# Kernel optimization log

Hardware: AMD Instinct MI355X
Metric: run time of the kernel (lower is better)

Reference implementation:

```python
import jax, jax.numpy as jnp
import numpy as np

N = 50000      # nodes
E = 800000     # edges
F_IN = 10      # node_feat_dim
H = 64         # hidden
ED = 3         # edge_dim
L = 3          # num_layers
EPS_LN = 1e-5


def _layernorm(x, g, b):
    mu = jnp.mean(x, axis=-1, keepdims=True)
    var = jnp.mean((x - mu) ** 2, axis=-1, keepdims=True)
    return (x - mu) * jax.lax.rsqrt(var + EPS_LN) * g + b


def setup_inputs() -> dict:
    key = jax.random.key(0)
    ks = jax.random.split(key, 20)
    x = jax.random.normal(ks[0], (N, F_IN), dtype=jnp.float32)
    edge_index = jax.random.randint(ks[1], (2, E), 0, N, dtype=jnp.int32)
    edge_attr = jax.random.uniform(ks[2], (E, ED), dtype=jnp.float32)

    def lin(k, fan_in, shape):
        return jax.random.normal(k, shape, dtype=jnp.float32) / np.sqrt(fan_in)

    params = {
        "Wp": lin(ks[3], F_IN, (F_IN, H)),
        "bp": jnp.zeros((H,), jnp.float32),
        # per-layer stacked params, leading dim L
        "ew1": lin(ks[4], ED, (L, ED, 16)),
        "eb1": jnp.zeros((L, 16), jnp.float32),
        "ew2": lin(ks[5], 16, (L, 16, 1)),
        "eb2": jnp.zeros((L, 1), jnp.float32),
        "nw": lin(ks[6], 2 * H, (L, 2 * H, H)),
        "nb": jnp.zeros((L, H), jnp.float32),
        "ln_g": jnp.ones((L, H), jnp.float32),
        "ln_b": jnp.zeros((L, H), jnp.float32),
        "hw1": lin(ks[7], H, (H, H // 2)),
        "hb1": jnp.zeros((H // 2,), jnp.float32),
        "hw2": lin(ks[8], H // 2, (H // 2, 1)),
        "hb2": jnp.zeros((1,), jnp.float32),
    }
    return {"x": x, "edge_index": edge_index, "edge_attr": edge_attr, **params}


def reference(x, edge_index, edge_attr, Wp, bp, ew1, eb1, ew2, eb2,
              nw, nb, ln_g, ln_b, hw1, hb1, hw2, hb2):
    src, dst = edge_index[0], edge_index[1]
    h = jax.nn.relu(x @ Wp + bp)                       # (N, H)
    for l in range(L):
        # edge MLP -> sigmoid weight per edge, shape (E, 1)
        ew = jax.nn.sigmoid(jax.nn.relu(edge_attr @ ew1[l] + eb1[l]) @ ew2[l] + eb2[l])
        msg = h[src] * ew                              # (E, H) gather + scale
        agg = jax.ops.segment_sum(msg, dst, num_segments=N)   # (N, H)
        cnt = jax.ops.segment_sum(ew, dst, num_segments=N)    # (N, 1)
        agg = agg / jnp.maximum(cnt, 1e-12)
        upd = jax.nn.relu(jnp.concatenate([h, agg], axis=1) @ nw[l] + nb[l])
        h = _layernorm(h + upd, ln_g[l], ln_b[l])
    return jax.nn.relu(h @ hw1 + hb1) @ hw2 + hb2      # (N, 1) logits
```

## Files before the change

kernel.cpp:

```cpp
#include <hip/hip_runtime.h>
#include <math.h>

#define N_NODES 50000
#define N_EDGES 800000
#define N_STRIPS 3125
#define N_BUCKETS 196
#define CAP_B 6144
#define CHUNK_A 2048
#define FILLA_BLOCKS 391
#define PROJ_BLOCKS 12500

typedef __attribute__((ext_vector_type(8))) short bf16x8;
typedef __attribute__((ext_vector_type(4))) float f32x4;
typedef __attribute__((ext_vector_type(2))) float f32x2;

__device__ __forceinline__ unsigned short f2bf(float f) {
  unsigned int u = __float_as_uint(f);
  u += 0x7FFFu + ((u >> 16) & 1u);
  return (unsigned short)(u >> 16);
}
__device__ __forceinline__ float bf2f(unsigned short s) {
  return __uint_as_float(((unsigned int)s) << 16);
}
__device__ __forceinline__ unsigned char f2fp8(float f) {
  return (unsigned char)(__builtin_amdgcn_cvt_pk_fp8_f32(f, f, 0, false) & 0xFF);
}

__global__ __launch_bounds__(256) void k_pre(const int* __restrict__ ei,
                                             const float* __restrict__ ea,
                                             const float* __restrict__ ew1,
                                             const float* __restrict__ eb1,
                                             const float* __restrict__ ew2,
                                             const float* __restrict__ eb2,
                                             int* __restrict__ bcur,
                                             uint2* __restrict__ buf1,
                                             const float* __restrict__ x,
                                             const float* __restrict__ Wp,
                                             const float* __restrict__ bp,
                                             unsigned short* __restrict__ hb,
                                             unsigned char* __restrict__ h8) {
  __shared__ int lcnt[N_BUCKETS];
  __shared__ int gb[N_BUCKETS];
  if (blockIdx.x >= FILLA_BLOCKS) {
    int idx = (blockIdx.x - FILLA_BLOCKS) * 256 + threadIdx.x;
    int n = idx >> 6, j = idx & 63;
    float acc = bp[j];
#pragma unroll
    for (int k = 0; k < 10; k++) acc += __builtin_nontemporal_load(&x[n * 10 + k]) * Wp[k * 64 + j];
    float r = fmaxf(acc, 0.f);
    hb[n * 64 + j] = f2bf(r);
    h8[n * 64 + j] = f2fp8(r);
    return;
  }
  for (int i = threadIdx.x; i < N_BUCKETS; i += 256) lcnt[i] = 0;
  __syncthreads();
  int base = blockIdx.x * CHUNK_A;
  uint2 rec[CHUNK_A / 256];
  int bk[CHUNK_A / 256], rk[CHUNK_A / 256];
#pragma unroll
  for (int k = 0; k < CHUNK_A / 256; k++) {
    int e = base + k * 256 + threadIdx.x;
    bk[k] = -1;
    if (e < N_EDGES) {
      int s = __builtin_nontemporal_load(&ei[e]);
      int d = __builtin_nontemporal_load(&ei[N_EDGES + e]);
      float a0 = __builtin_nontemporal_load(&ea[e * 3 + 0]);
      float a1 = __builtin_nontemporal_load(&ea[e * 3 + 1]);
      float a2 = __builtin_nontemporal_load(&ea[e * 3 + 2]);
      int q[3];
#pragma unroll
      for (int l = 0; l < 3; l++) {
        float z = eb2[l];
#pragma unroll
        for (int t = 0; t < 16; t++) {
          float hd = a0 * ew1[l * 48 + t] + a1 * ew1[l * 48 + 16 + t] +
                     a2 * ew1[l * 48 + 32 + t] + eb1[l * 16 + t];
          z += fmaxf(hd, 0.f) * ew2[l * 16 + t];
        }
        float w = 1.f / (1.f + __expf(-z));
        q[l] = __float2int_rn(w * 8191.f);
      }
      unsigned int dl = (unsigned int)(d & 255);
      rec[k].x = (unsigned int)s | ((unsigned int)q[0] << 17) | ((dl & 3u) << 30);
      rec[k].y = (unsigned int)q[1] | ((unsigned int)q[2] << 13) | ((dl >> 2) << 26);
      int b = d >> 8;
      bk[k] = b;
      rk[k] = atomicAdd(&lcnt[b], 1);
    }
  }
  __syncthreads();
  if (threadIdx.x < N_BUCKETS) {
    int c = lcnt[threadIdx.x];
    gb[threadIdx.x] = threadIdx.x * CAP_B + (c ? atomicAdd(&bcur[threadIdx.x], c) : 0);
  }
  __syncthreads();
#pragma unroll
  for (int k = 0; k < CHUNK_A / 256; k++)
    if (bk[k] >= 0) buf1[gb[bk[k]] + rk[k]] = rec[k];
}

__global__ __launch_bounds__(256) void k_fillB(const uint2* __restrict__ buf1,
                                               const int* __restrict__ bcur,
                                               uint2* __restrict__ csr,
                                               int* __restrict__ aoffs,
                                               int* __restrict__ adeg,
                                               int* __restrict__ order) {
  __shared__ int lhist[256];
  __shared__ int lscan[256];
  __shared__ int lcls[8];
  __shared__ int lbase[8];
  int b = blockIdx.x;
  int t = threadIdx.x;
  int segbase = b * CAP_B;
  int cnt = bcur[b];
  lhist[t] = 0;
  if (t < 8) lcls[t] = 0;
  __syncthreads();
  for (int i = t; i < cnt; i += 256) {
    uint2 rec = buf1[segbase + i];
    int dl = (int)((rec.x >> 30) | (((rec.y >> 26) & 63u) << 2));
    atomicAdd(&lhist[dl], 1);
  }
  __syncthreads();
  int v = lhist[t];
  lscan[t] = v;
  __syncthreads();
#pragma unroll
  for (int off = 1; off < 256; off <<= 1) {
    int u = (t >= off) ? lscan[t - off] : 0;
    __syncthreads();
    lscan[t] += u;
    __syncthreads();
  }
  int excl = lscan[t] - v;
  int nid = b * 256 + t;
  int cls = 0, rank = 0;
  bool valid = nid < N_NODES;
  if (valid) {
    aoffs[nid] = segbase + excl;
    adeg[nid] = v;
    cls = min(v >> 2, 7);
    rank = atomicAdd(&lcls[cls], 1);
  }
  __syncthreads();
  if (t == 0) {
    int acc2 = 0;
#pragma unroll
    for (int c = 0; c < 8; c++) { lbase[c] = acc2; acc2 += lcls[c]; }
  }
  lhist[t] = segbase + excl;
  __syncthreads();
  if (valid) order[b * 256 + lbase[cls] + rank] = nid;
  for (int i = t; i < cnt; i += 256) {
    uint2 rec = buf1[segbase + i];
    int dl = (int)((rec.x >> 30) | (((rec.y >> 26) & 63u) << 2));
    int pos = atomicAdd(&lhist[dl], 1);
    csr[pos] = rec;
  }
}

template <int LI>
__device__ __forceinline__ float decw(uint2 c) {
  unsigned int q = (LI == 0) ? ((c.x >> 17) & 0x1FFFu)
                 : (LI == 1) ? (c.y & 0x1FFFu)
                             : ((c.y >> 13) & 0x1FFFu);
  return (float)q * (1.f / 8191.f);
}

template <int LI>
__global__ __launch_bounds__(256, 8) void k_agg(const uint2* __restrict__ csr,
                                                const int* __restrict__ aoffs,
                                                const int* __restrict__ adeg,
                                                const int* __restrict__ order,
                                                const unsigned char* __restrict__ h8in,
                                                unsigned short* __restrict__ ab) {
  int lane = threadIdx.x & 63;
  int sub = lane >> 3;
  int jj = lane & 7;
  int gw = (blockIdx.x * 256 + threadIdx.x) >> 6;
  int idx = gw * 8 + sub;
  bool active = idx < N_NODES;
  int n = active ? order[idx] : 0;
  int start = active ? aoffs[n] : 0;
  int d = active ? adeg[n] : 0;
  const uint2* hrow = (const uint2*)h8in;
  float a0 = 0.f, a1 = 0.f, a2 = 0.f, a3 = 0.f;
  float a4 = 0.f, a5 = 0.f, a6 = 0.f, a7 = 0.f, ws = 0.f;
  int i = 0;
  if (d >= 4) {
    uint2 c0 = csr[start + 0], c1 = csr[start + 1];
    uint2 c2 = csr[start + 2], c3 = csr[start + 3];
    for (;;) {
      int nxt = i + 4;
      bool more = (nxt + 4 <= d);
      uint2 m0, m1, m2, m3;
      if (more) {
        m0 = csr[start + nxt + 0]; m1 = csr[start + nxt + 1];
        m2 = csr[start + nxt + 2]; m3 = csr[start + nxt + 3];
      }
      uint2 g0 = hrow[(c0.x & 0x1FFFFu) * 8 + jj];
      uint2 g1 = hrow[(c1.x & 0x1FFFFu) * 8 + jj];
      uint2 g2 = hrow[(c2.x & 0x1FFFFu) * 8 + jj];
      uint2 g3 = hrow[(c3.x & 0x1FFFFu) * 8 + jj];
      float w0 = decw<LI>(c0), w1 = decw<LI>(c1), w2 = decw<LI>(c2), w3 = decw<LI>(c3);
#pragma unroll
      for (int k = 0; k < 4; k++) {
        uint2 g = (k == 0) ? g0 : (k == 1) ? g1 : (k == 2) ? g2 : g3;
        float w = (k == 0) ? w0 : (k == 1) ? w1 : (k == 2) ? w2 : w3;
        f32x2 p01 = __builtin_amdgcn_cvt_pk_f32_fp8(g.x, false);
        f32x2 p23 = __builtin_amdgcn_cvt_pk_f32_fp8(g.x, true);
        f32x2 p45 = __builtin_amdgcn_cvt_pk_f32_fp8(g.y, false);
        f32x2 p67 = __builtin_amdgcn_cvt_pk_f32_fp8(g.y, true);
        a0 += p01[0] * w; a1 += p01[1] * w;
        a2 += p23[0] * w; a3 += p23[1] * w;
        a4 += p45[0] * w; a5 += p45[1] * w;
        a6 += p67[0] * w; a7 += p67[1] * w;
      }
      ws += w0 + w1 + w2 + w3;
      i = nxt;
      if (!more) break;
      c0 = m0; c1 = m1; c2 = m2; c3 = m3;
    }
  }
  for (; i < d; ++i) {
    uint2 c = csr[start + i];
    uint2 g = hrow[(c.x & 0x1FFFFu) * 8 + jj];
    float w = decw<LI>(c);
    f32x2 p01 = __builtin_amdgcn_cvt_pk_f32_fp8(g.x, false);
    f32x2 p23 = __builtin_amdgcn_cvt_pk_f32_fp8(g.x, true);
    f32x2 p45 = __builtin_amdgcn_cvt_pk_f32_fp8(g.y, false);
    f32x2 p67 = __builtin_amdgcn_cvt_pk_f32_fp8(g.y, true);
    a0 += p01[0] * w; a1 += p01[1] * w;
    a2 += p23[0] * w; a3 += p23[1] * w;
    a4 += p45[0] * w; a5 += p45[1] * w;
    a6 += p67[0] * w; a7 += p67[1] * w;
    ws += w;
  }
  if (active) {
    float inv = 1.f / fmaxf(ws, 1e-12f);
    uint4 o;
    o.x = (unsigned int)f2bf(a0 * inv) | ((unsigned int)f2bf(a1 * inv) << 16);
    o.y = (unsigned int)f2bf(a2 * inv) | ((unsigned int)f2bf(a3 * inv) << 16);
    o.z = (unsigned int)f2bf(a4 * inv) | ((unsigned int)f2bf(a5 * inv) << 16);
    o.w = (unsigned int)f2bf(a6 * inv) | ((unsigned int)f2bf(a7 * inv) << 16);
    ((uint4*)ab)[n * 8 + jj] = o;
  }
}

template <bool HEAD>
__global__ __launch_bounds__(256) void k_mlp(const float* __restrict__ nw,
                                             const float* __restrict__ nb,
                                             const float* __restrict__ g,
                                             const float* __restrict__ b,
                                             const unsigned short* __restrict__ hb_in,
                                             const unsigned short* __restrict__ ab_in,
                                             unsigned short* __restrict__ hbout,
                                             unsigned char* __restrict__ h8out,
                                             const float* __restrict__ hw1,
                                             const float* __restrict__ hb1,
                                             const float* __restrict__ hw2,
                                             const float* __restrict__ hb2,
                                             float* __restrict__ out) {
  __shared__ unsigned short lh[4][16 * 72];
  int lane = threadIdx.x & 63;
  int n16 = lane & 15;
  int q = lane >> 4;
  int wv = threadIdx.x >> 6;
  int wid = (blockIdx.x * 256 + threadIdx.x) >> 6;
  int nwaves = gridDim.x * 4;

  bf16x8 bfr[4][4];
#pragma unroll
  for (int t = 0; t < 4; t++)
#pragma unroll
    for (int kc = 0; kc < 4; kc++) {
      bf16x8 v;
#pragma unroll
      for (int jj = 0; jj < 8; jj++) {
        int k = kc * 32 + q * 8 + jj;
        v[jj] = (short)f2bf(nw[k * 64 + t * 16 + n16]);
      }
      bfr[t][kc] = v;
    }
  bf16x8 eye[2];
#pragma unroll
  for (int p = 0; p < 2; p++) {
    bf16x8 v;
#pragma unroll
    for (int jj = 0; jj < 8; jj++)
      v[jj] = ((q * 8 + jj) == (n16 + 16 * p)) ? (short)0x3F80 : (short)0;
    eye[p] = v;
  }
  float nbv[4], gv[4], bv[4];
#pragma unroll
  for (int t = 0; t < 4; t++) {
    nbv[t] = nb[t * 16 + n16];
    gv[t] = g[t * 16 + n16];
    bv[t] = b[t * 16 + n16];
  }
  bf16x8 hfr[2][2];
  float hb1v[2], hw2v[2], hb2v = 0.f;
  if (HEAD) {
#pragma unroll
    for (int kc = 0; kc < 2; kc++)
#pragma unroll
      for (int tl = 0; tl < 2; tl++) {
        bf16x8 v;
#pragma unroll
        for (int jj = 0; jj < 8; jj++)
          v[jj] = (short)f2bf(hw1[(kc * 32 + q * 8 + jj) * 32 + tl * 16 + n16]);
        hfr[kc][tl] = v;
      }
#pragma unroll
    for (int tl = 0; tl < 2; tl++) {
      hb1v[tl] = hb1[tl * 16 + n16];
      hw2v[tl] = hw2[tl * 16 + n16];
    }
    hb2v = hb2[0];
  }

  for (int s = wid; s < N_STRIPS; s += nwaves) {
    int n0 = s * 16;
    f32x4 acc[4] = {{0.f, 0.f, 0.f, 0.f}, {0.f, 0.f, 0.f, 0.f},
                    {0.f, 0.f, 0.f, 0.f}, {0.f, 0.f, 0.f, 0.f}};
    bf16x8 afr[4];
#pragma unroll
    for (int kc = 0; kc < 4; kc++) {
      const unsigned short* base = (kc < 2) ? hb_in : ab_in;
      afr[kc] = __builtin_nontemporal_load(
          (const bf16x8*)(base + (size_t)(n0 + n16) * 64 + (kc & 1) * 32 + q * 8));
#pragma unroll
      for (int t = 0; t < 4; t++)
        acc[t] = __builtin_amdgcn_mfma_f32_16x16x32_bf16(afr[kc], bfr[t][kc], acc[t], 0, 0, 0);
    }
    f32x4 rres[4];
#pragma unroll
    for (int t = 0; t < 4; t++) {
      f32x4 z = {0.f, 0.f, 0.f, 0.f};
      rres[t] = __builtin_amdgcn_mfma_f32_16x16x32_bf16(afr[t >> 1], eye[t & 1], z, 0, 0, 0);
    }
    float r[4][4];
    float p[4], p2[4];
#pragma unroll
    for (int rg = 0; rg < 4; rg++) { p[rg] = 0.f; p2[rg] = 0.f; }
#pragma unroll
    for (int t = 0; t < 4; t++)
#pragma unroll
      for (int rg = 0; rg < 4; rg++) {
        float rr = rres[t][rg] + fmaxf(acc[t][rg] + nbv[t], 0.f);
        r[t][rg] = rr;
        p[rg] += rr;
        p2[rg] += rr * rr;
      }
#pragma unroll
    for (int rg = 0; rg < 4; rg++)
#pragma unroll
      for (int off = 1; off < 16; off <<= 1) {
        p[rg] += __shfl_xor(p[rg], off);
        p2[rg] += __shfl_xor(p2[rg], off);
      }
#pragma unroll
    for (int rg = 0; rg < 4; rg++) {
      float mu = p[rg] * (1.f / 64.f);
      float var = p2[rg] * (1.f / 64.f) - mu * mu;
      float rs = rsqrtf(fmaxf(var, 0.f) + 1e-5f);
      int row = n0 + q * 4 + rg;
#pragma unroll
      for (int t = 0; t < 4; t++) {
        float o = (r[t][rg] - mu) * rs * gv[t] + bv[t];
        unsigned short ob = f2bf(o);
        hbout[row * 64 + t * 16 + n16] = ob;
        h8out[row * 64 + t * 16 + n16] = f2fp8(o);
        if (HEAD) lh[wv][(q * 4 + rg) * 72 + t * 16 + n16] = ob;
      }
    }
    if (HEAD) {
      asm volatile("s_waitcnt lgkmcnt(0)" ::: "memory");
      f32x4 hacc[2] = {{0.f, 0.f, 0.f, 0.f}, {0.f, 0.f, 0.f, 0.f}};
#pragma unroll
      for (int kc = 0; kc < 2; kc++) {
        bf16x8 ha = *(const bf16x8*)&lh[wv][n16 * 72 + kc * 32 + q * 8];
#pragma unroll
        for (int tl = 0; tl < 2; tl++)
          hacc[tl] = __builtin_amdgcn_mfma_f32_16x16x32_bf16(ha, hfr[kc][tl], hacc[tl], 0, 0, 0);
      }
#pragma unroll
      for (int rg = 0; rg < 4; rg++) {
        float sres = fmaxf(hacc[0][rg] + hb1v[0], 0.f) * hw2v[0] +
                     fmaxf(hacc[1][rg] + hb1v[1], 0.f) * hw2v[1];
#pragma unroll
        for (int off = 1; off < 16; off <<= 1) sres += __shfl_xor(sres, off);
        if (n16 == 0) out[n0 + q * 4 + rg] = sres + hb2v;
      }
    }
  }
}

static inline size_t align256(size_t x) { return (x + 255) & ~size_t(255); }

extern "C" void kernel_launch(void* const* d_in, const int* in_sizes, int n_in,
                              void* d_out, int out_size, void* d_ws, size_t ws_size,
                              hipStream_t stream) {
  const float* x   = (const float*)d_in[0];
  const int*   ei  = (const int*)d_in[1];
  const float* ea  = (const float*)d_in[2];
  const float* Wp  = (const float*)d_in[3];
  const float* bp  = (const float*)d_in[4];
  const float* ew1 = (const float*)d_in[5];
  const float* eb1 = (const float*)d_in[6];
  const float* ew2 = (const float*)d_in[7];
  const float* eb2 = (const float*)d_in[8];
  const float* nw  = (const float*)d_in[9];
  const float* nb  = (const float*)d_in[10];
  const float* lng = (const float*)d_in[11];
  const float* lnb = (const float*)d_in[12];
  const float* hw1 = (const float*)d_in[13];
  const float* hb1 = (const float*)d_in[14];
  const float* hw2 = (const float*)d_in[15];
  const float* hb2 = (const float*)d_in[16];
  float* out = (float*)d_out;

  char* ws = (char*)d_ws;
  size_t off = 0;
  unsigned short* hb0  = (unsigned short*)(ws + off); off = align256(off + (size_t)N_NODES * 64 * 2);
  unsigned short* hb1b = (unsigned short*)(ws + off); off = align256(off + (size_t)N_NODES * 64 * 2);
  unsigned short* ab   = (unsigned short*)(ws + off); off = align256(off + (size_t)N_NODES * 64 * 2);
  unsigned char* h8_0  = (unsigned char*)(ws + off); off = align256(off + (size_t)N_NODES * 64);
  unsigned char* h8_1  = (unsigned char*)(ws + off); off = align256(off + (size_t)N_NODES * 64);
  uint2* csr  = (uint2*)(ws + off); off = align256(off + (size_t)N_BUCKETS * CAP_B * 8);
  uint2* buf1 = (uint2*)(ws + off); off = align256(off + (size_t)N_BUCKETS * CAP_B * 8);
  int* aoffs  = (int*)(ws + off); off = align256(off + (size_t)N_NODES * 4);
  int* adeg   = (int*)(ws + off); off = align256(off + (size_t)N_NODES * 4);
  int* order  = (int*)(ws + off); off = align256(off + (size_t)N_NODES * 4);
  int* bcur   = (int*)(ws + off); off = align256(off + 1024);

  (void)hipMemsetAsync(bcur, 0, N_BUCKETS * 4, stream);
  k_pre<<<FILLA_BLOCKS + PROJ_BLOCKS, 256, 0, stream>>>(ei, ea, ew1, eb1, ew2, eb2, bcur, buf1,
                                                        x, Wp, bp, hb0, h8_0);
  k_fillB<<<N_BUCKETS, 256, 0, stream>>>(buf1, bcur, csr, aoffs, adeg, order);

  const int aggGrid = (N_NODES + 31) / 32;
  const int mlpGrid = 392;

  k_agg<0><<<aggGrid, 256, 0, stream>>>(csr, aoffs, adeg, order, h8_0, ab);
  k_mlp<false><<<mlpGrid, 256, 0, stream>>>(nw + 0 * 8192, nb + 0 * 64, lng + 0 * 64, lnb + 0 * 64,
                                            hb0, ab, hb1b, h8_1, hw1, hb1, hw2, hb2, out);
  k_agg<1><<<aggGrid, 256, 0, stream>>>(csr, aoffs, adeg, order, h8_1, ab);
  k_mlp<false><<<mlpGrid, 256, 0, stream>>>(nw + 1 * 8192, nb + 1 * 64, lng + 1 * 64, lnb + 1 * 64,
                                            hb1b, ab, hb0, h8_0, hw1, hb1, hw2, hb2, out);
  k_agg<2><<<aggGrid, 256, 0, stream>>>(csr, aoffs, adeg, order, h8_0, ab);
  k_mlp<true><<<mlpGrid, 256, 0, stream>>>(nw + 2 * 8192, nb + 2 * 64, lng + 2 * 64, lnb + 2 * 64,
                                           hb0, ab, hb1b, h8_1, hw1, hb1, hw2, hb2, out);
}
```

Before: 220.6 us.

## Fuse neighbor aggregation into node-update MLP kernel and split CSR per layer

Merges the per-layer aggregation kernel and the MLP/LayerNorm kernel into one persistent kernel. Each wave aggregates 16 degree-sorted nodes into shared memory and feeds them straight into the MFMA update, which removes the bf16 aggregate round trip through global memory and half the launches. The CSR records are also repacked into three 4-byte per-layer arrays (source index plus that layer's quantized weight) instead of one 8-byte record, halving edge-stream bytes per layer. In exchange, node rows are now read and written in degree-sorted scattered order, and occupancy is limited by the launch bound of 3 blocks.

```diff
diff --git a/kernel.cpp b/kernel.cpp
--- a/kernel.cpp
+++ b/kernel.cpp
@@ -18,9 +18,6 @@
   unsigned int u = __float_as_uint(f);
   u += 0x7FFFu + ((u >> 16) & 1u);
   return (unsigned short)(u >> 16);
-}
-__device__ __forceinline__ float bf2f(unsigned short s) {
-  return __uint_as_float(((unsigned int)s) << 16);
 }
 __device__ __forceinline__ unsigned char f2fp8(float f) {
   return (unsigned char)(__builtin_amdgcn_cvt_pk_fp8_f32(f, f, 0, false) & 0xFF);
@@ -101,7 +98,9 @@
 
 __global__ __launch_bounds__(256) void k_fillB(const uint2* __restrict__ buf1,
                                                const int* __restrict__ bcur,
-                                               uint2* __restrict__ csr,
+                                               unsigned int* __restrict__ pl0,
+                                               unsigned int* __restrict__ pl1,
+                                               unsigned int* __restrict__ pl2,
                                                int* __restrict__ aoffs,
                                                int* __restrict__ adeg,
                                                int* __restrict__ order) {
@@ -155,180 +154,170 @@
     uint2 rec = buf1[segbase + i];
     int dl = (int)((rec.x >> 30) | (((rec.y >> 26) & 63u) << 2));
     int pos = atomicAdd(&lhist[dl], 1);
-    csr[pos] = rec;
-  }
-}
-
-template <int LI>
-__device__ __forceinline__ float decw(uint2 c) {
-  unsigned int q = (LI == 0) ? ((c.x >> 17) & 0x1FFFu)
-                 : (LI == 1) ? (c.y & 0x1FFFu)
-                             : ((c.y >> 13) & 0x1FFFu);
-  return (float)q * (1.f / 8191.f);
-}
-
-template <int LI>
-__global__ __launch_bounds__(256, 8) void k_agg(const uint2* __restrict__ csr,
-                                                const int* __restrict__ aoffs,
-                                                const int* __restrict__ adeg,
-                                                const int* __restrict__ order,
-                                                const unsigned char* __restrict__ h8in,
-                                                unsigned short* __restrict__ ab) {
+    unsigned int src = rec.x & 0x1FFFFu;
+    pl0[pos] = src | ((rec.x >> 17) & 0x1FFFu) << 17;
+    pl1[pos] = src | (rec.y & 0x1FFFu) << 17;
+    pl2[pos] = src | ((rec.y >> 13) & 0x1FFFu) << 17;
+  }
+}
+
+template <bool HEAD>
+__global__ __launch_bounds__(256, 3) void k_layer(
+    const unsigned int* __restrict__ pl,
+    const int* __restrict__ aoffs,
+    const int* __restrict__ adeg,
+    const int* __restrict__ order,
+    const unsigned char* __restrict__ h8in,
+    const unsigned short* __restrict__ hb_in,
+    const float* __restrict__ nw, const float* __restrict__ nb,
+    const float* __restrict__ g, const float* __restrict__ b,
+    unsigned short* __restrict__ hbout, unsigned char* __restrict__ h8out,
+    const float* __restrict__ hw1, const float* __restrict__ hb1,
+    const float* __restrict__ hw2, const float* __restrict__ hb2,
+    float* __restrict__ out) {
+  __shared__ unsigned short lt[4][16 * 72];
   int lane = threadIdx.x & 63;
+  int n16 = lane & 15;
+  int q = lane >> 4;
   int sub = lane >> 3;
   int jj = lane & 7;
-  int gw = (blockIdx.x * 256 + threadIdx.x) >> 6;
-  int idx = gw * 8 + sub;
-  bool active = idx < N_NODES;
-  int n = active ? order[idx] : 0;
-  int start = active ? aoffs[n] : 0;
-  int d = active ? adeg[n] : 0;
+  int wv = threadIdx.x >> 6;
+  int wid = (blockIdx.x * 256 + threadIdx.x) >> 6;
+  int nwaves = gridDim.x * 4;
+
+  bf16x8 bfr[4][4];
+#pragma unroll
+  for (int t = 0; t < 4; t++)
+#pragma unroll
+    for (int kc = 0; kc < 4; kc++) {
+      bf16x8 v;
+#pragma unroll
+      for (int j2 = 0; j2 < 8; j2++) {
+        int k = kc * 32 + q * 8 + j2;
+        v[j2] = (short)f2bf(nw[k * 64 + t * 16 + n16]);
+      }
+      bfr[t][kc] = v;
+    }
+  bf16x8 eye[2];
+#pragma unroll
+  for (int p = 0; p < 2; p++) {
+    bf16x8 v;
+#pragma unroll
+    for (int j2 = 0; j2 < 8; j2++)
+      v[j2] = ((q * 8 + j2) == (n16 + 16 * p)) ? (short)0x3F80 : (short)0;
+    eye[p] = v;
+  }
+  float nbv[4], gv[4], bv[4];
+#pragma unroll
+  for (int t = 0; t < 4; t++) {
+    nbv[t] = nb[t * 16 + n16];
+    gv[t] = g[t * 16 + n16];
+    bv[t] = b[t * 16 + n16];
+  }
+  bf16x8 hfr[2][2];
+  float hb1v[2], hw2v[2], hb2v = 0.f;
+  if (HEAD) {
+#pragma unroll
+    for (int kc = 0; kc < 2; kc++)
+#pragma unroll
+      for (int tl = 0; tl < 2; tl++) {
+        bf16x8 v;
+#pragma unroll
+        for (int j2 = 0; j2 < 8; j2++)
+          v[j2] = (short)f2bf(hw1[(kc * 32 + q * 8 + j2) * 32 + tl * 16 + n16]);
+        hfr[kc][tl] = v;
+      }
+#pragma unroll
+    for (int tl = 0; tl < 2; tl++) {
+      hb1v[tl] = hb1[tl * 16 + n16];
+      hw2v[tl] = hw2[tl * 16 + n16];
+    }
+    hb2v = hb2[0];
+  }
+
   const uint2* hrow = (const uint2*)h8in;
-  float a0 = 0.f, a1 = 0.f, a2 = 0.f, a3 = 0.f;
-  float a4 = 0.f, a5 = 0.f, a6 = 0.f, a7 = 0.f, ws = 0.f;
-  int i = 0;
-  if (d >= 4) {
-    uint2 c0 = csr[start + 0], c1 = csr[start + 1];
-    uint2 c2 = csr[start + 2], c3 = csr[start + 3];
-    for (;;) {
-      int nxt = i + 4;
-      bool more = (nxt + 4 <= d);
-      uint2 m0, m1, m2, m3;
-      if (more) {
-        m0 = csr[start + nxt + 0]; m1 = csr[start + nxt + 1];
-        m2 = csr[start + nxt + 2]; m3 = csr[start + nxt + 3];
-      }
-      uint2 g0 = hrow[(c0.x & 0x1FFFFu) * 8 + jj];
-      uint2 g1 = hrow[(c1.x & 0x1FFFFu) * 8 + jj];
-      uint2 g2 = hrow[(c2.x & 0x1FFFFu) * 8 + jj];
-      uint2 g3 = hrow[(c3.x & 0x1FFFFu) * 8 + jj];
-      float w0 = decw<LI>(c0), w1 = decw<LI>(c1), w2 = decw<LI>(c2), w3 = decw<LI>(c3);
-#pragma unroll
-      for (int k = 0; k < 4; k++) {
-        uint2 g = (k == 0) ? g0 : (k == 1) ? g1 : (k == 2) ? g2 : g3;
-        float w = (k == 0) ? w0 : (k == 1) ? w1 : (k == 2) ? w2 : w3;
-        f32x2 p01 = __builtin_amdgcn_cvt_pk_f32_fp8(g.x, false);
-        f32x2 p23 = __builtin_amdgcn_cvt_pk_f32_fp8(g.x, true);
-        f32x2 p45 = __builtin_amdgcn_cvt_pk_f32_fp8(g.y, false);
-        f32x2 p67 = __builtin_amdgcn_cvt_pk_f32_fp8(g.y, true);
+
+  for (int s = wid; s < N_STRIPS; s += nwaves) {
+#pragma unroll
+    for (int half = 0; half < 2; half++) {
+      int n = order[s * 16 + half * 8 + sub];
+      int start = aoffs[n];
+      int d = adeg[n];
+      float a0 = 0.f, a1 = 0.f, a2 = 0.f, a3 = 0.f;
+      float a4 = 0.f, a5 = 0.f, a6 = 0.f, a7 = 0.f, ws = 0.f;
+      int i = 0;
+      if (d >= 4) {
+        unsigned int c0 = pl[start + 0], c1 = pl[start + 1];
+        unsigned int c2 = pl[start + 2], c3 = pl[start + 3];
+        for (;;) {
+          int nxt = i + 4;
+          bool more = (nxt + 4 <= d);
+          unsigned int m0, m1, m2, m3;
+          if (more) {
+            m0 = pl[start + nxt + 0]; m1 = pl[start + nxt + 1];
+            m2 = pl[start + nxt + 2]; m3 = pl[start + nxt + 3];
+          }
+          uint2 g0 = hrow[(c0 & 0x1FFFFu) * 8 + jj];
+          uint2 g1 = hrow[(c1 & 0x1FFFFu) * 8 + jj];
+          uint2 g2 = hrow[(c2 & 0x1FFFFu) * 8 + jj];
+          uint2 g3 = hrow[(c3 & 0x1FFFFu) * 8 + jj];
+          float w0 = (float)(c0 >> 17) * (1.f / 8191.f);
+          float w1 = (float)(c1 >> 17) * (1.f / 8191.f);
+          float w2 = (float)(c2 >> 17) * (1.f / 8191.f);
+          float w3 = (float)(c3 >> 17) * (1.f / 8191.f);
+#pragma unroll
+          for (int k = 0; k < 4; k++) {
+            uint2 gg = (k == 0) ? g0 : (k == 1) ? g1 : (k == 2) ? g2 : g3;
+            float w = (k == 0) ? w0 : (k == 1) ? w1 : (k == 2) ? w2 : w3;
+            f32x2 p01 = __builtin_amdgcn_cvt_pk_f32_fp8(gg.x, false);
+            f32x2 p23 = __builtin_amdgcn_cvt_pk_f32_fp8(gg.x, true);
+            f32x2 p45 = __builtin_amdgcn_cvt_pk_f32_fp8(gg.y, false);
+            f32x2 p67 = __builtin_amdgcn_cvt_pk_f32_fp8(gg.y, true);
+            a0 += p01[0] * w; a1 += p01[1] * w;
+            a2 += p23[0] * w; a3 += p23[1] * w;
+            a4 += p45[0] * w; a5 += p45[1] * w;
+            a6 += p67[0] * w; a7 += p67[1] * w;
+          }
+          ws += w0 + w1 + w2 + w3;
+          i = nxt;
+          if (!more) break;
+          c0 = m0; c1 = m1; c2 = m2; c3 = m3;
+        }
+      }
+      for (; i < d; ++i) {
+        unsigned int c = pl[start + i];
+        uint2 gg = hrow[(c & 0x1FFFFu) * 8 + jj];
+        float w = (float)(c >> 17) * (1.f / 8191.f);
+        f32x2 p01 = __builtin_amdgcn_cvt_pk_f32_fp8(gg.x, false);
+        f32x2 p23 = __builtin_amdgcn_cvt_pk_f32_fp8(gg.x, true);
+        f32x2 p45 = __builtin_amdgcn_cvt_pk_f32_fp8(gg.y, false);
+        f32x2 p67 = __builtin_amdgcn_cvt_pk_f32_fp8(gg.y, true);
         a0 += p01[0] * w; a1 += p01[1] * w;
         a2 += p23[0] * w; a3 += p23[1] * w;
         a4 += p45[0] * w; a5 += p45[1] * w;
         a6 += p67[0] * w; a7 += p67[1] * w;
-      }
-      ws += w0 + w1 + w2 + w3;
-      i = nxt;
-      if (!more) break;
-      c0 = m0; c1 = m1; c2 = m2; c3 = m3;
-    }
-  }
-  for (; i < d; ++i) {
-    uint2 c = csr[start + i];
-    uint2 g = hrow[(c.x & 0x1FFFFu) * 8 + jj];
-    float w = decw<LI>(c);
-    f32x2 p01 = __builtin_amdgcn_cvt_pk_f32_fp8(g.x, false);
-    f32x2 p23 = __builtin_amdgcn_cvt_pk_f32_fp8(g.x, true);
-    f32x2 p45 = __builtin_amdgcn_cvt_pk_f32_fp8(g.y, false);
-    f32x2 p67 = __builtin_amdgcn_cvt_pk_f32_fp8(g.y, true);
-    a0 += p01[0] * w; a1 += p01[1] * w;
-    a2 += p23[0] * w; a3 += p23[1] * w;
-    a4 += p45[0] * w; a5 += p45[1] * w;
-    a6 += p67[0] * w; a7 += p67[1] * w;
-    ws += w;
-  }
-  if (active) {
-    float inv = 1.f / fmaxf(ws, 1e-12f);
-    uint4 o;
-    o.x = (unsigned int)f2bf(a0 * inv) | ((unsigned int)f2bf(a1 * inv) << 16);
-    o.y = (unsigned int)f2bf(a2 * inv) | ((unsigned int)f2bf(a3 * inv) << 16);
-    o.z = (unsigned int)f2bf(a4 * inv) | ((unsigned int)f2bf(a5 * inv) << 16);
-    o.w = (unsigned int)f2bf(a6 * inv) | ((unsigned int)f2bf(a7 * inv) << 16);
-    ((uint4*)ab)[n * 8 + jj] = o;
-  }
-}
-
-template <bool HEAD>
-__global__ __launch_bounds__(256) void k_mlp(const float* __restrict__ nw,
-                                             const float* __restrict__ nb,
-                                             const float* __restrict__ g,
-                                             const float* __restrict__ b,
-                                             const unsigned short* __restrict__ hb_in,
-                                             const unsigned short* __restrict__ ab_in,
-                                             unsigned short* __restrict__ hbout,
-                                             unsigned char* __restrict__ h8out,
-                                             const float* __restrict__ hw1,
-                                             const float* __restrict__ hb1,
-                                             const float* __restrict__ hw2,
-                                             const float* __restrict__ hb2,
-                                             float* __restrict__ out) {
-  __shared__ unsigned short lh[4][16 * 72];
-  int lane = threadIdx.x & 63;
-  int n16 = lane & 15;
-  int q = lane >> 4;
-  int wv = threadIdx.x >> 6;
-  int wid = (blockIdx.x * 256 + threadIdx.x) >> 6;
-  int nwaves = gridDim.x * 4;
-
-  bf16x8 bfr[4][4];
-#pragma unroll
-  for (int t = 0; t < 4; t++)
-#pragma unroll
-    for (int kc = 0; kc < 4; kc++) {
-      bf16x8 v;
-#pragma unroll
-      for (int jj = 0; jj < 8; jj++) {
-        int k = kc * 32 + q * 8 + jj;
-        v[jj] = (short)f2bf(nw[k * 64 + t * 16 + n16]);
-      }
-      bfr[t][kc] = v;
-    }
-  bf16x8 eye[2];
-#pragma unroll
-  for (int p = 0; p < 2; p++) {
-    bf16x8 v;
-#pragma unroll
-    for (int jj = 0; jj < 8; jj++)
-      v[jj] = ((q * 8 + jj) == (n16 + 16 * p)) ? (short)0x3F80 : (short)0;
-    eye[p] = v;
-  }
-  float nbv[4], gv[4], bv[4];
-#pragma unroll
-  for (int t = 0; t < 4; t++) {
-    nbv[t] = nb[t * 16 + n16];
-    gv[t] = g[t * 16 + n16];
-    bv[t] = b[t * 16 + n16];
-  }
-  bf16x8 hfr[2][2];
-  float hb1v[2], hw2v[2], hb2v = 0.f;
-  if (HEAD) {
-#pragma unroll
-    for (int kc = 0; kc < 2; kc++)
-#pragma unroll
-      for (int tl = 0; tl < 2; tl++) {
-        bf16x8 v;
-#pragma unroll
-        for (int jj = 0; jj < 8; jj++)
-          v[jj] = (short)f2bf(hw1[(kc * 32 + q * 8 + jj) * 32 + tl * 16 + n16]);
-        hfr[kc][tl] = v;
-      }
-#pragma unroll
-    for (int tl = 0; tl < 2; tl++) {
-      hb1v[tl] = hb1[tl * 16 + n16];
-      hw2v[tl] = hw2[tl * 16 + n16];
-    }
-    hb2v = hb2[0];
-  }
-
-  for (int s = wid; s < N_STRIPS; s += nwaves) {
-    int n0 = s * 16;
+        ws += w;
+      }
+      float inv = 1.f / fmaxf(ws, 1e-12f);
+      unsigned int u0 = (unsigned int)f2bf(a0 * inv) | ((unsigned int)f2bf(a1 * inv) << 16);
+      unsigned int u1 = (unsigned int)f2bf(a2 * inv) | ((unsigned int)f2bf(a3 * inv) << 16);
+      unsigned int u2 = (unsigned int)f2bf(a4 * inv) | ((unsigned int)f2bf(a5 * inv) << 16);
+      unsigned int u3 = (unsigned int)f2bf(a6 * inv) | ((unsigned int)f2bf(a7 * inv) << 16);
+      unsigned int* dst = (unsigned int*)&lt[wv][(half * 8 + sub) * 72 + jj * 8];
+      dst[0] = u0; dst[1] = u1; dst[2] = u2; dst[3] = u3;
+    }
+    asm volatile("s_waitcnt lgkmcnt(0)" ::: "memory");
+    int ordn = order[s * 16 + n16];
     f32x4 acc[4] = {{0.f, 0.f, 0.f, 0.f}, {0.f, 0.f, 0.f, 0.f},
                     {0.f, 0.f, 0.f, 0.f}, {0.f, 0.f, 0.f, 0.f}};
     bf16x8 afr[4];
 #pragma unroll
     for (int kc = 0; kc < 4; kc++) {
-      const unsigned short* base = (kc < 2) ? hb_in : ab_in;
-      afr[kc] = __builtin_nontemporal_load(
-          (const bf16x8*)(base + (size_t)(n0 + n16) * 64 + (kc & 1) * 32 + q * 8));
+      if (kc < 2)
+        afr[kc] = __builtin_nontemporal_load(
+            (const bf16x8*)(hb_in + (size_t)ordn * 64 + (kc & 1) * 32 + q * 8));
+      else
+        afr[kc] = *(const bf16x8*)&lt[wv][n16 * 72 + (kc & 1) * 32 + q * 8];
 #pragma unroll
       for (int t = 0; t < 4; t++)
         acc[t] = __builtin_amdgcn_mfma_f32_16x16x32_bf16(afr[kc], bfr[t][kc], acc[t], 0, 0, 0);
@@ -359,19 +348,22 @@
         p[rg] += __shfl_xor(p[rg], off);
         p2[rg] += __shfl_xor(p2[rg], off);
       }
+    int rnode[4];
+#pragma unroll
+    for (int rg = 0; rg < 4; rg++) rnode[rg] = order[s * 16 + q * 4 + rg];
 #pragma unroll
     for (int rg = 0; rg < 4; rg++) {
       float mu = p[rg] * (1.f / 64.f);
       float var = p2[rg] * (1.f / 64.f) - mu * mu;
       float rs = rsqrtf(fmaxf(var, 0.f) + 1e-5f);
-      int row = n0 + q * 4 + rg;
+      int row = rnode[rg];
 #pragma unroll
       for (int t = 0; t < 4; t++) {
         float o = (r[t][rg] - mu) * rs * gv[t] + bv[t];
         unsigned short ob = f2bf(o);
         hbout[row * 64 + t * 16 + n16] = ob;
         h8out[row * 64 + t * 16 + n16] = f2fp8(o);
-        if (HEAD) lh[wv][(q * 4 + rg) * 72 + t * 16 + n16] = ob;
+        if (HEAD) lt[wv][(q * 4 + rg) * 72 + t * 16 + n16] = ob;
       }
     }
     if (HEAD) {
@@ -379,7 +371,7 @@
       f32x4 hacc[2] = {{0.f, 0.f, 0.f, 0.f}, {0.f, 0.f, 0.f, 0.f}};
 #pragma unroll
       for (int kc = 0; kc < 2; kc++) {
-        bf16x8 ha = *(const bf16x8*)&lh[wv][n16 * 72 + kc * 32 + q * 8];
+        bf16x8 ha = *(const bf16x8*)&lt[wv][n16 * 72 + kc * 32 + q * 8];
 #pragma unroll
         for (int tl = 0; tl < 2; tl++)
           hacc[tl] = __builtin_amdgcn_mfma_f32_16x16x32_bf16(ha, hfr[kc][tl], hacc[tl], 0, 0, 0);
@@ -390,7 +382,7 @@
                      fmaxf(hacc[1][rg] + hb1v[1], 0.f) * hw2v[1];
 #pragma unroll
         for (int off = 1; off < 16; off <<= 1) sres += __shfl_xor(sres, off);
-        if (n16 == 0) out[n0 + q * 4 + rg] = sres + hb2v;
+        if (n16 == 0) out[rnode[rg]] = sres + hb2v;
       }
     }
   }
@@ -424,11 +416,12 @@
   size_t off = 0;
   unsigned short* hb0  = (unsigned short*)(ws + off); off = align256(off + (size_t)N_NODES * 64 * 2);
   unsigned short* hb1b = (unsigned short*)(ws + off); off = align256(off + (size_t)N_NODES * 64 * 2);
-  unsigned short* ab   = (unsigned short*)(ws + off); off = align256(off + (size_t)N_NODES * 64 * 2);
   unsigned char* h8_0  = (unsigned char*)(ws + off); off = align256(off + (size_t)N_NODES * 64);
   unsigned char* h8_1  = (unsigned char*)(ws + off); off = align256(off + (size_t)N_NODES * 64);
-  uint2* csr  = (uint2*)(ws + off); off = align256(off + (size_t)N_BUCKETS * CAP_B * 8);
   uint2* buf1 = (uint2*)(ws + off); off = align256(off + (size_t)N_BUCKETS * CAP_B * 8);
+  unsigned int* pl0 = (unsigned int*)(ws + off); off = align256(off + (size_t)N_BUCKETS * CAP_B * 4);
+  unsigned int* pl1 = (unsigned int*)(ws + off); off = align256(off + (size_t)N_BUCKETS * CAP_B * 4);
+  unsigned int* pl2 = (unsigned int*)(ws + off); off = align256(off + (size_t)N_BUCKETS * CAP_B * 4);
   int* aoffs  = (int*)(ws + off); off = align256(off + (size_t)N_NODES * 4);
   int* adeg   = (int*)(ws + off); off = align256(off + (size_t)N_NODES * 4);
   int* order  = (int*)(ws + off); off = align256(off + (size_t)N_NODES * 4);
@@ -437,18 +430,17 @@
   (void)hipMemsetAsync(bcur, 0, N_BUCKETS * 4, stream);
   k_pre<<<FILLA_BLOCKS + PROJ_BLOCKS, 256, 0, stream>>>(ei, ea, ew1, eb1, ew2, eb2, bcur, buf1,
                                                         x, Wp, bp, hb0, h8_0);
-  k_fillB<<<N_BUCKETS, 256, 0, stream>>>(buf1, bcur, csr, aoffs, adeg, order);
-
-  const int aggGrid = (N_NODES + 31) / 32;
-  const int mlpGrid = 392;
-
-  k_agg<0><<<aggGrid, 256, 0, stream>>>(csr, aoffs, adeg, order, h8_0, ab);
-  k_mlp<false><<<mlpGrid, 256, 0, stream>>>(nw + 0 * 8192, nb + 0 * 64, lng + 0 * 64, lnb + 0 * 64,
-                                            hb0, ab, hb1b, h8_1, hw1, hb1, hw2, hb2, out);
-  k_agg<1><<<aggGrid, 256, 0, stream>>>(csr, aoffs, adeg, order, h8_1, ab);
-  k_mlp<false><<<mlpGrid, 256, 0, stream>>>(nw + 1 * 8192, nb + 1 * 64, lng + 1 * 64, lnb + 1 * 64,
-                                            hb1b, ab, hb0, h8_0, hw1, hb1, hw2, hb2, out);
-  k_agg<2><<<aggGrid, 256, 0, stream>>>(csr, aoffs, adeg, order, h8_0, ab);
-  k_mlp<true><<<mlpGrid, 256, 0, stream>>>(nw + 2 * 8192, nb + 2 * 64, lng + 2 * 64, lnb + 2 * 64,
-                                           hb0, ab, hb1b, h8_1, hw1, hb1, hw2, hb2, out);
-}
+  k_fillB<<<N_BUCKETS, 256, 0, stream>>>(buf1, bcur, pl0, pl1, pl2, aoffs, adeg, order);
+
+  const int layerGrid = 782;
+
+  k_layer<false><<<layerGrid, 256, 0, stream>>>(pl0, aoffs, adeg, order, h8_0, hb0,
+                                                nw + 0 * 8192, nb + 0 * 64, lng + 0 * 64, lnb + 0 * 64,
+                                                hb1b, h8_1, hw1, hb1, hw2, hb2, out);
+  k_layer<false><<<layerGrid, 256, 0, stream>>>(pl1, aoffs, adeg, order, h8_1, hb1b,
+                                                nw + 1 * 8192, nb + 1 * 64, lng + 1 * 64, lnb + 1 * 64,
+                                                hb0, h8_0, hw1, hb1, hw2, hb2, out);
+  k_layer<true><<<layerGrid, 256, 0, stream>>>(pl2, aoffs, adeg, order, h8_0, hb0,
+                                               nw + 2 * 8192, nb + 2 * 64, lng + 2 * 64, lnb + 2 * 64,
+                                               hb1b, h8_1, hw1, hb1, hw2, hb2, out);
+}
```

Result: slower. 249.7 us (+13.2%).
